# Optimization experiments

Measured on AMD Instinct MI355X. Metric: run time of the kernel, lower is better.

The kernel has to match this reference:

```python
import jax, jax.numpy as jnp
import numpy as np

N, E, G = 100000, 3200000, 5000
EPS = 1e-5
HEADS, HC = 8, 16


def setup_inputs() -> dict:
    key = jax.random.key(0)
    k = jax.random.split(key, 12)

    def lin(kk, fi, fo):
        return (jax.random.normal(kk, (fi, fo), jnp.float32) / np.sqrt(fi)).astype(jnp.float32)

    return {
        "x": jax.random.normal(k[0], (N, 20), jnp.float32),
        "edge_index": jax.random.randint(k[1], (2, E), 0, N, dtype=jnp.int32),
        "batch": jnp.sort(jax.random.randint(k[2], (N,), 0, G, dtype=jnp.int32)),
        "W1": lin(k[3], 20, 64), "b1": jnp.zeros((64,), jnp.float32),
        "g1": jnp.ones((64,), jnp.float32), "be1": jnp.zeros((64,), jnp.float32),
        "W2": lin(k[4], 64, 32), "b2": jnp.zeros((32,), jnp.float32),
        "g2": jnp.ones((32,), jnp.float32), "be2": jnp.zeros((32,), jnp.float32),
        "W3": lin(k[5], 32, 16), "b3": jnp.zeros((16,), jnp.float32),
        "g3": jnp.ones((16,), jnp.float32), "be3": jnp.zeros((16,), jnp.float32),
        "Wg": lin(k[6], 16, HEADS * HC),
        "att_src": jax.random.normal(k[7], (HEADS, HC), jnp.float32) * 0.1,
        "att_dst": jax.random.normal(k[8], (HEADS, HC), jnp.float32) * 0.1,
        "bg": jnp.zeros((HC,), jnp.float32),
        "Wf": lin(k[9], 16, 3), "bf": jnp.zeros((3,), jnp.float32),
    }


def reference(x, edge_index, batch,
              W1, b1, g1, be1, W2, b2, g2, be2, W3, b3, g3, be3,
              Wg, att_src, att_dst, bg, Wf, bf):
    src, dst = edge_index[0], edge_index[1]
    loop = jnp.arange(N, dtype=src.dtype)
    src_sl = jnp.concatenate([src, loop])  # self-loops (GCN + GAT add_self_loops)
    dst_sl = jnp.concatenate([dst, loop])

    # GCN symmetric normalization D^-1/2 (A+I) D^-1/2
    deg = jax.ops.segment_sum(jnp.ones_like(src_sl, dtype=jnp.float32), dst_sl, N)
    dinv = jnp.where(deg > 0, 1.0 / jnp.sqrt(deg), 0.0)
    norm = (dinv[src_sl] * dinv[dst_sl])[:, None]  # [E+N, 1]

    def gcn(h, W, b):
        h = h @ W
        return jax.ops.segment_sum(h[src_sl] * norm, dst_sl, N) + b

    def bn_relu(h, g, b):  # BatchNorm1d (train-mode batch stats) + ReLU
        mu = h.mean(0)
        var = ((h - mu) ** 2).mean(0)
        return jax.nn.relu(g * (h - mu) * jax.lax.rsqrt(var + EPS) + b)

    h = bn_relu(gcn(x, W1, b1), g1, be1)   # dropout = identity (eval)
    h = bn_relu(gcn(h, W2, b2), g2, be2)
    h = bn_relu(gcn(h, W3, b3), g3, be3)

    # GATConv: heads=8, concat=False (mean over heads), eval -> no dropout
    xg = (h @ Wg).reshape(N, HEADS, HC)
    a_src = (xg * att_src).sum(-1)  # [N, H]
    a_dst = (xg * att_dst).sum(-1)
    logit = jax.nn.leaky_relu(a_src[src_sl] + a_dst[dst_sl], 0.2)  # [E+N, H]
    m = jax.ops.segment_max(logit, dst_sl, N)          # segment softmax over dst
    e = jnp.exp(logit - m[dst_sl])
    s = jax.ops.segment_sum(e, dst_sl, N)
    alpha = e / s[dst_sl]
    agg = jax.ops.segment_sum(xg[src_sl] * alpha[:, :, None], dst_sl, N)  # [N,H,C]
    hg = agg.mean(1) + bg  # [N, 16]

    pooled = jax.ops.segment_sum(hg, batch, G)  # global_add_pool -> [G, 16]
    return pooled @ Wf + bf  # [G, 3]
```

## Files before the change

### kernel.cpp

```cpp
#include <hip/hip_runtime.h>
#include <hip/hip_fp16.h>

constexpr int NN = 100000;
constexpr int EE = 3200000;
constexpr int GG = 5000;
constexpr float BNEPS = 1e-5f;

constexpr int BINS = 128;
constexpr int NPB = (NN + BINS - 1) / BINS;
constexpr int BCHUNK = 8192;
constexpr int NBCH = (EE + BCHUNK - 1) / BCHUNK;
constexpr int BINCAP2 = 96;
constexpr int BINREG = 27648;
constexpr int LCAP = 26624;
constexpr int CTR_STRIDE = 32;

typedef int int4v __attribute__((ext_vector_type(4)));



__global__ __launch_bounds__(1024) void bin_edges(const int* __restrict__ ei,
                                                  unsigned* __restrict__ pairs,
                                                  int* __restrict__ binCur) {
    __shared__ int bcnt[BINS];
    __shared__ int bbase[BINS];
    __shared__ unsigned buf[BINS][BINCAP2];
    const int t = threadIdx.x;
    const int lane = t & 63, wv = t >> 6;
    for (int ch = blockIdx.x; ch < NBCH; ch += gridDim.x) {
        for (int k = t; k < BINS; k += 1024) bcnt[k] = 0;
        __syncthreads();
        const int qbase = ch * (BCHUNK / 4);
#pragma unroll
        for (int rep = 0; rep < 2; ++rep) {
            const int q = qbase + rep * 1024 + t;
            if (q < EE / 4) {
                int4v d = __builtin_nontemporal_load((const int4v*)(ei + EE) + q);
                int4v s = __builtin_nontemporal_load((const int4v*)ei + q);
                int dd[4] = {d.x, d.y, d.z, d.w};
                int ss[4] = {s.x, s.y, s.z, s.w};
#pragma unroll
                for (int k = 0; k < 4; ++k) {
                    int o = dd[k] / NPB;
                    unsigned pk = ((unsigned)(dd[k] - o * NPB) << 17) | (unsigned)ss[k];
                    int p = atomicAdd(&bcnt[o], 1);
                    if (p < BINCAP2) {
                        buf[o][p] = pk;
                    } else {
                        int gp = atomicAdd(&binCur[o * CTR_STRIDE], 1);
                        pairs[(size_t)o * BINREG + gp] = pk;
                    }
                }
            }
        }
        __syncthreads();
        if (t < BINS) {
            int c = bcnt[t] < BINCAP2 ? bcnt[t] : BINCAP2;
            bbase[t] = atomicAdd(&binCur[t * CTR_STRIDE], c);
            bcnt[t] = c;
        }
        __syncthreads();
        for (int o = wv; o < BINS; o += 16) {
            const int c = bcnt[o];
            const size_t base = (size_t)o * BINREG + bbase[o];
            for (int k = lane; k < c; k += 64) pairs[base + k] = buf[o][k];
        }
        __syncthreads();
    }
}


__global__ void bin_base(const int* __restrict__ binCur, int* __restrict__ binBase) {
    __shared__ int s[BINS];
    const int t = threadIdx.x;
    const int v = binCur[t * CTR_STRIDE];
    s[t] = v;
    __syncthreads();
    for (int off = 1; off < BINS; off <<= 1) {
        int add = (t >= off) ? s[t - off] : 0;
        __syncthreads();
        s[t] += add;
        __syncthreads();
    }
    binBase[t] = s[t] - v;
}


__global__ __launch_bounds__(1024) void scatter_lds(const unsigned* __restrict__ pairs,
                                                    const int* __restrict__ binCur,
                                                    const int* __restrict__ binBase,
                                                    int* __restrict__ rowptr,
                                                    float* __restrict__ dinv,
                                                    int* __restrict__ colA) {
    __shared__ int scnt[NPB];
    __shared__ int sscan[1024];
    __shared__ int lbuf[LCAP];
    const int b = blockIdx.x;
    const int t = threadIdx.x;
    const int lo = b * NPB;
    const int hi = (lo + NPB < NN) ? lo + NPB : NN;
    const int nb = hi - lo;
    const int tot = binCur[b * CTR_STRIDE];
    const int base = binBase[b];
    const unsigned* p = pairs + (size_t)b * BINREG;
    for (int k = t; k < nb; k += 1024) scnt[k] = 0;
    __syncthreads();
    for (int q = t; q < tot; q += 1024) atomicAdd(&scnt[p[q] >> 17], 1);
    __syncthreads();
    const int myc = (t < nb) ? scnt[t] : 0;
    sscan[t] = myc;
    __syncthreads();
    for (int off = 1; off < 1024; off <<= 1) {
        int add = (t >= off) ? sscan[t - off] : 0;
        __syncthreads();
        sscan[t] += add;
        __syncthreads();
    }
    const int excl = sscan[t] - myc;
    if (t < nb) {
        rowptr[lo + t] = base + excl;
        dinv[lo + t] = rsqrtf((float)(myc + 1));
        scnt[t] = excl;
    }
    if (b == BINS - 1 && t == 0) rowptr[NN] = base + tot;
    __syncthreads();
    for (int q = t; q < tot; q += 1024) {
        unsigned e = p[q];
        int pos = atomicAdd(&scnt[e >> 17], 1);
        int src = (int)(e & 0x1FFFFu);
        if (pos < LCAP) lbuf[pos] = src;
        else colA[base + pos] = src;
    }
    __syncthreads();
    const int m = tot < LCAP ? tot : LCAP;
    for (int k = t; k < m; k += 1024) colA[base + k] = lbuf[k];
}


__global__ void scale_x(const float* __restrict__ x, const float* __restrict__ dinv,
                        __half* __restrict__ xsc) {
    int idx = blockIdx.x * blockDim.x + threadIdx.x;
    if (idx < NN * 20) {
        int n = idx / 20;
        xsc[idx] = __float2half(x[idx] * dinv[n]);
    }
}


template <int FIN, int FOUT, bool AFFINE, bool SCALED, bool STATS, bool DUAL, bool SPLITOUT>
__global__ void gemm_k(const __half* __restrict__ hinA, const __half* __restrict__ hinB,
                       const float* __restrict__ sumsIn, const float* __restrict__ ssqIn,
                       const float* __restrict__ g, const float* __restrict__ be,
                       const float* __restrict__ W, const float* __restrict__ dinv,
                       const float* __restrict__ bias,
                       __half* __restrict__ outA, __half* __restrict__ outB,
                       float* __restrict__ sumsOut, float* __restrict__ ssqOut) {
    constexpr int NB = 256 / FOUT;
    __shared__ float Wl[FIN * FOUT];
    __shared__ float rows[NB][FIN];
    __shared__ float aa[AFFINE ? FIN : 1], bb[AFFINE ? FIN : 1];
    const int t = threadIdx.x;
    if constexpr (AFFINE) {
        if (t < FIN) {
            float mu = sumsIn[t] / (float)NN;
            float var = ssqIn[t] / (float)NN - mu * mu;
            float a = g[t] * rsqrtf(var + BNEPS);
            aa[t] = a;
            bb[t] = be[t] - mu * a;
        }
    }
    for (int i = t; i < FIN * FOUT; i += 256) Wl[i] = W[i];
    const int c = t % FOUT, s = t / FOUT;
    const int ngrp = (NN + NB - 1) / NB;
    float sAcc = 0.f, qAcc = 0.f;
    for (int grp = blockIdx.x; grp < ngrp; grp += gridDim.x) {
        __syncthreads();
        for (int i = t; i < NB * FIN; i += 256) {
            int sn = i / FIN, k = i % FIN;
            int n2 = grp * NB + sn;
            float v = 0.f;
            if (n2 < NN) {
                __half hv;
                if constexpr (DUAL) {
                    hv = (k < FIN / 2) ? hinA[(size_t)n2 * (FIN / 2) + k]
                                       : hinB[(size_t)n2 * (FIN / 2) + k - FIN / 2];
                } else {
                    hv = hinA[(size_t)n2 * FIN + k];
                }
                v = __half2float(hv);
                if constexpr (AFFINE) {
                    v = aa[k] * v + bb[k];
                    v = v > 0.f ? v : 0.f;
                }
            }
            rows[sn][k] = v;
        }
        __syncthreads();
        int node = grp * NB + s;
        if (node < NN) {
            float acc = 0.f;
#pragma unroll
            for (int k = 0; k < FIN; ++k) acc += rows[s][k] * Wl[k * FOUT + c];
            if constexpr (SCALED) {
                __half hv = __float2half(acc * dinv[node]);
                if constexpr (SPLITOUT) {
                    ((c < FOUT / 2) ? outA : outB)[(size_t)node * (FOUT / 2) + (c % (FOUT / 2))] = hv;
                } else {
                    outA[(size_t)node * FOUT + c] = hv;
                }
            } else {
                float val = acc + bias[c];
                outA[(size_t)node * FOUT + c] = __float2half(val);
                if constexpr (STATS) { sAcc += val; qAcc += val * val; }
            }
        }
    }
    if constexpr (STATS) {
        __shared__ float ls[FOUT], lq[FOUT];
        __syncthreads();
        if (t < FOUT) { ls[t] = 0.f; lq[t] = 0.f; }
        __syncthreads();
        atomicAdd(&ls[c], sAcc);
        atomicAdd(&lq[c], qAcc);
        __syncthreads();
        if (t < FOUT) { atomicAdd(&sumsOut[t], ls[t]); atomicAdd(&ssqOut[t], lq[t]); }
    }
}


template <int H2, int OUTF, bool STATS>
__global__ void agg_half(const __half2* __restrict__ src, const int* __restrict__ rowptr,
                         const int* __restrict__ colA, const float* __restrict__ dinv,
                         const float* __restrict__ bias, __half* __restrict__ out,
                         float* __restrict__ sumsOut, float* __restrict__ ssqOut) {
    constexpr int SUB = 64 / H2;
    const int lane = threadIdx.x & 63;
    const int wid = (blockIdx.x * blockDim.x + threadIdx.x) >> 6;
    const int totalWaves = (gridDim.x * blockDim.x) >> 6;
    const int f = lane % H2;
    const int sub = lane / H2;
    const int stride = totalWaves * SUB;
    float bx = 0.f, by = 0.f;
    if (bias != nullptr) {
        bx = bias[2 * f];
        by = bias[2 * f + 1];
    }
    const int i0 = (sub < SUB) ? wid * SUB + sub : NN;
    float sx = 0.f, qx = 0.f, sy = 0.f, qy = 0.f;
    for (int i = i0; i < NN; i += stride) {
        const int r0 = rowptr[i], r1 = rowptr[i + 1];
        float2 acc = __half22float2(src[(size_t)i * H2 + f]);
        float2 acc2 = {0.f, 0.f};
        int e = r0;
        for (; e + 3 < r1; e += 4) {
            int j0 = colA[e], j1 = colA[e + 1], j2 = colA[e + 2], j3 = colA[e + 3];
            float2 v0 = __half22float2(src[(size_t)j0 * H2 + f]);
            float2 v1 = __half22float2(src[(size_t)j1 * H2 + f]);
            float2 v2 = __half22float2(src[(size_t)j2 * H2 + f]);
            float2 v3 = __half22float2(src[(size_t)j3 * H2 + f]);
            acc.x += v0.x + v1.x;
            acc.y += v0.y + v1.y;
            acc2.x += v2.x + v3.x;
            acc2.y += v2.y + v3.y;
        }
        for (; e < r1; ++e) {
            float2 v = __half22float2(src[(size_t)colA[e] * H2 + f]);
            acc.x += v.x; acc.y += v.y;
        }
        acc.x += acc2.x; acc.y += acc2.y;
        const float d = dinv[i];
        float vx = d * acc.x + bx;
        float vy = d * acc.y + by;
        *(__half2*)(out + (size_t)i * OUTF + 2 * f) = __floats2half2_rn(vx, vy);
        if constexpr (STATS) { sx += vx; qx += vx * vx; sy += vy; qy += vy * vy; }
    }
    if constexpr (STATS) {
        __shared__ float ls[OUTF], lq[OUTF];
        const int t = threadIdx.x;
        if (t < OUTF) { ls[t] = 0.f; lq[t] = 0.f; }
        __syncthreads();
        atomicAdd(&ls[2 * f], sx);
        atomicAdd(&lq[2 * f], qx);
        atomicAdd(&ls[2 * f + 1], sy);
        atomicAdd(&lq[2 * f + 1], qy);
        __syncthreads();
        if (t < OUTF) { atomicAdd(&sumsOut[t], ls[t]); atomicAdd(&ssqOut[t], lq[t]); }
    }
}


__global__ void gat_mats(const float* __restrict__ Wg, const float* __restrict__ att_src,
                         const float* __restrict__ att_dst, const float* __restrict__ Wf,
                         const float* __restrict__ bg, float* __restrict__ Psrc,
                         float* __restrict__ Pdst, float* __restrict__ M,
                         float* __restrict__ bgW) {
    int t = threadIdx.x;
    if (t < 128) {
        int k = t >> 3, h = t & 7;
        float s = 0.f, d = 0.f;
        for (int c = 0; c < 16; ++c) {
            float wv = Wg[k * 128 + h * 16 + c];
            s += wv * att_src[h * 16 + c];
            d += wv * att_dst[h * 16 + c];
        }
        Psrc[k * 8 + h] = s;
        Pdst[k * 8 + h] = d;
    } else if (t < 512) {
        int m = t - 128;
        if (m < 384) {
            int hk = m / 3, j = m - hk * 3;
            int H = hk >> 4, k = hk & 15;
            float s = 0.f;
            for (int c = 0; c < 16; ++c) s += Wg[k * 128 + H * 16 + c] * Wf[c * 3 + j];
            M[hk * 3 + j] = 0.125f * s;
        }
    } else if (t < 515) {
        int j = t - 512;
        float s = 0.f;
        for (int c = 0; c < 16; ++c) s += bg[c] * Wf[c * 3 + j];
        bgW[j] = s;
    }
}


__global__ void gat_pre2(const __half* __restrict__ h3,
                         const float* __restrict__ sums3, const float* __restrict__ ssq3,
                         const float* __restrict__ g3, const float* __restrict__ be3,
                         const float* __restrict__ Psrc, const float* __restrict__ Pdst,
                         float4* __restrict__ zas, float* __restrict__ adst) {
    __shared__ float Ps[128], Pd[128], aa[16], bb[16];
    int t = threadIdx.x;
    if (t < 128) { Ps[t] = Psrc[t]; Pd[t] = Pdst[t]; }
    if (t < 16) {
        float mu = sums3[t] / (float)NN;
        float var = ssq3[t] / (float)NN - mu * mu;
        float a = g3[t] * rsqrtf(var + BNEPS);
        aa[t] = a;
        bb[t] = be3[t] - mu * a;
    }
    __syncthreads();
    int n = blockIdx.x * blockDim.x + t;
    if (n >= NN) return;
    union { float4 f4[2]; __half2 h2v[8]; } u;
    const float4* hp = (const float4*)(h3 + (size_t)n * 16);
    u.f4[0] = hp[0];
    u.f4[1] = hp[1];
    float zv[16];
#pragma unroll
    for (int k = 0; k < 8; ++k) {
        float2 p = __half22float2(u.h2v[k]);
        float v0 = aa[2 * k] * p.x + bb[2 * k];
        float v1 = aa[2 * k + 1] * p.y + bb[2 * k + 1];
        zv[2 * k] = v0 > 0.f ? v0 : 0.f;
        zv[2 * k + 1] = v1 > 0.f ? v1 : 0.f;
    }
    __half2 zh[8];
#pragma unroll
    for (int k = 0; k < 8; ++k) zh[k] = __floats2half2_rn(zv[2 * k], zv[2 * k + 1]);
    float as[8], ad[8];
#pragma unroll
    for (int h = 0; h < 8; ++h) { as[h] = 0.f; ad[h] = 0.f; }
#pragma unroll
    for (int k = 0; k < 16; ++k) {
        float zk = zv[k];
#pragma unroll
        for (int h = 0; h < 8; ++h) {
            as[h] += zk * Ps[k * 8 + h];
            ad[h] += zk * Pd[k * 8 + h];
        }
    }
    float4* zrow = zas + (size_t)n * 4;
    zrow[0] = ((float4*)zh)[0];
    zrow[1] = ((float4*)zh)[1];
    zrow[2] = make_float4(as[0], as[1], as[2], as[3]);
    zrow[3] = make_float4(as[4], as[5], as[6], as[7]);
    float4* d4 = (float4*)(adst + (size_t)n * 8);
    d4[0] = make_float4(ad[0], ad[1], ad[2], ad[3]);
    d4[1] = make_float4(ad[4], ad[5], ad[6], ad[7]);
}


__device__ __forceinline__ float leaky02(float x) { return x > 0.f ? x : 0.2f * x; }

__global__ void gat_agg7(const float4* __restrict__ zas, const float* __restrict__ adst,
                         const int* __restrict__ rowptr, const int* __restrict__ colA,
                         const int* __restrict__ batch, const float* __restrict__ Mg,
                         float* __restrict__ out) {
    __shared__ float Ml[384];
    for (int k = threadIdx.x; k < 384; k += 256) Ml[k] = Mg[k];
    __syncthreads();
    const int lane = threadIdx.x & 63;
    const int ls = lane & 7;
    const int q = ls & 3;
    const int hh = ls >> 2;
    const int grp = lane >> 3;
    const int gb = lane & 56;
    const int wid = (blockIdx.x * blockDim.x + threadIdx.x) >> 6;
    const int totalWaves = (gridDim.x * blockDim.x) >> 6;
    const int stride = totalWaves * 8;
    const char* zb = (const char*)zas;
    for (int i = wid * 8 + grp; i < NN; i += stride) {
        const int r0 = rowptr[i], r1 = rowptr[i + 1];
        const float adv = __builtin_nontemporal_load(adst + (size_t)i * 8 + ls);
        float acc[4][4];
        float wsum[4];
#pragma unroll
        for (int h = 0; h < 4; ++h) {
            wsum[h] = 0.f;
#pragma unroll
            for (int k = 0; k < 4; ++k) acc[h][k] = 0.f;
        }
        auto compute = [&](float av, float2 zr, bool val) {
            const __half2* zp = (const __half2*)&zr;
            const float2 f0 = __half22float2(zp[0]), f1 = __half22float2(zp[1]);
            const float zf[4] = {f0.x, f0.y, f1.x, f1.y};
            const float w = val ? __expf(leaky02(av + adv)) : 0.f;
            float wq[4];
#pragma unroll
            for (int h = 0; h < 4; ++h) wq[h] = __shfl(w, gb + hh * 4 + h);
#pragma unroll
            for (int h = 0; h < 4; ++h) {
                wsum[h] += wq[h];
#pragma unroll
                for (int k = 0; k < 4; ++k) acc[h][k] += wq[h] * zf[k];
            }
        };
        int e = r0;
        int jA = i, jB = i;
        bool vB = false;
        if (e < r1) { jB = colA[e]; ++e; vB = true; }
        const char* rowA = zb + (size_t)jA * 64;
        const char* rowB = zb + (size_t)jB * 64;
        float avA = *(const float*)(rowA + 32 + ls * 4);
        float2 zA = *(const float2*)(rowA + q * 8);
        float avB = *(const float*)(rowB + 32 + ls * 4);
        float2 zB = *(const float2*)(rowB + q * 8);
        while (true) {
            int jA2 = i, jB2 = i;
            bool vA2 = false, vB2 = false;
            if (e < r1) { jA2 = colA[e]; ++e; vA2 = true; }
            if (e < r1) { jB2 = colA[e]; ++e; vB2 = true; }
            const char* rA2 = zb + (size_t)jA2 * 64;
            const char* rB2 = zb + (size_t)jB2 * 64;
            float avA2 = *(const float*)(rA2 + 32 + ls * 4);
            float2 zA2 = *(const float2*)(rA2 + q * 8);
            float avB2 = *(const float*)(rB2 + 32 + ls * 4);
            float2 zB2 = *(const float2*)(rB2 + q * 8);
            compute(avA, zA, true);
            compute(avB, zB, vB);
            if (!vA2) break;
            avA = avA2; zA = zA2; avB = avB2; zB = zB2; vB = vB2;
        }
        float o0 = 0.f, o1 = 0.f, o2 = 0.f;
#pragma unroll
        for (int h = 0; h < 4; ++h) {
            const float inv = 1.f / wsum[h];
            const int hk0 = (hh * 4 + h) * 16 + q * 4;
#pragma unroll
            for (int k = 0; k < 4; ++k) {
                const float v = acc[h][k] * inv;
                const float* m = &Ml[(hk0 + k) * 3];
                o0 += v * m[0];
                o1 += v * m[1];
                o2 += v * m[2];
            }
        }
#pragma unroll
        for (int off = 1; off < 8; off <<= 1) {
            o0 += __shfl_xor(o0, off);
            o1 += __shfl_xor(o1, off);
            o2 += __shfl_xor(o2, off);
        }
        const int g = batch[i];
        if (ls < 3) {
            const float ov = (ls == 0) ? o0 : (ls == 1) ? o1 : o2;
            atomicAdd(&out[g * 3 + ls], ov);
        }
    }
}


__global__ void graph_bounds(const int* __restrict__ batch, int* __restrict__ gstart) {
    int n = blockIdx.x * blockDim.x + threadIdx.x;
    if (n < NN) {
        int bn = batch[n];
        int bp = (n == 0) ? -1 : batch[n - 1];
        for (int g = bp + 1; g <= bn; ++g) gstart[g] = n;
        if (n == NN - 1)
            for (int g = bn + 1; g <= GG; ++g) gstart[g] = NN;
    }
}


__global__ void pool_init(const int* __restrict__ gstart, const float* __restrict__ bgW,
                          const float* __restrict__ bf, float* __restrict__ out) {
    int g = blockIdx.x * blockDim.x + threadIdx.x;
    if (g < GG) {
        float cnt = (float)(gstart[g + 1] - gstart[g]);
#pragma unroll
        for (int j = 0; j < 3; ++j) out[g * 3 + j] = cnt * bgW[j] + bf[j];
    }
}


extern "C" void kernel_launch(void* const* d_in, const int* in_sizes, int n_in,
                              void* d_out, int out_size, void* d_ws, size_t ws_size,
                              hipStream_t stream) {
    const float* x = (const float*)d_in[0];
    const int* ei = (const int*)d_in[1];
    const int* batch = (const int*)d_in[2];
    const float* W1 = (const float*)d_in[3];  const float* b1 = (const float*)d_in[4];
    const float* g1 = (const float*)d_in[5];  const float* be1 = (const float*)d_in[6];
    const float* W2 = (const float*)d_in[7];  const float* b2 = (const float*)d_in[8];
    const float* g2 = (const float*)d_in[9];  const float* be2 = (const float*)d_in[10];
    const float* W3 = (const float*)d_in[11]; const float* b3 = (const float*)d_in[12];
    const float* g3 = (const float*)d_in[13]; const float* be3 = (const float*)d_in[14];
    const float* Wg = (const float*)d_in[15];
    const float* att_src = (const float*)d_in[16];
    const float* att_dst = (const float*)d_in[17];
    const float* bg = (const float*)d_in[18];
    const float* Wf = (const float*)d_in[19];
    const float* bf = (const float*)d_in[20];
    float* out = (float*)d_out;

    char* w = (char*)d_ws;
    auto alloc = [&](size_t bytes) -> char* {
        char* p = w;
        w += (bytes + 255) & ~(size_t)255;
        return p;
    };
    int* binCur = (int*)alloc((size_t)BINS * CTR_STRIDE * 4);
    float* sums1 = (float*)alloc(64 * 4); float* ssq1 = (float*)alloc(64 * 4);
    float* sums2 = (float*)alloc(32 * 4); float* ssq2 = (float*)alloc(32 * 4);
    float* sums3 = (float*)alloc(16 * 4); float* ssq3 = (float*)alloc(16 * 4);
    size_t zeroBytes = (size_t)(w - (char*)d_ws);
    int* binBase = (int*)alloc((size_t)BINS * 4);
    float* Psrc = (float*)alloc(128 * 4);
    float* Pdst = (float*)alloc(128 * 4);
    float* Mm = (float*)alloc(384 * 4);
    float* bgW = (float*)alloc(3 * 4);
    int* gstart = (int*)alloc((size_t)(GG + 1) * 4);
    int* rowptr = (int*)alloc((size_t)(NN + 1) * 4);
    int* colA = (int*)alloc((size_t)EE * 4);
    float* dinv = (float*)alloc((size_t)NN * 4);
    char* A = alloc((size_t)NN * 64 * 4);
    char* B = alloc((size_t)NN * 64 * 4);

    unsigned* pairs = (unsigned*)A;
    __half* xsc  = (__half*)B;
    __half* aggx = (__half*)(B + (size_t)NN * 64);
    __half* h1   = (__half*)A;
    __half* hs2a = (__half*)B;
    __half* hs2b = (__half*)(B + (size_t)NN * 32);
    __half* h2a  = (__half*)(B + (size_t)NN * 64);
    __half* h2b  = (__half*)(B + (size_t)NN * 96);
    __half* hs3  = (__half*)A;
    __half* h3   = (__half*)(A + (size_t)NN * 32);
    char*   zas  = A + (size_t)NN * 96;
    float*  adst = (float*)(A + (size_t)NN * 160);

    hipMemsetAsync(d_ws, 0, zeroBytes, stream);

    bin_edges<<<256, 1024, 0, stream>>>(ei, pairs, binCur);
    bin_base<<<1, BINS, 0, stream>>>(binCur, binBase);
    scatter_lds<<<BINS, 1024, 0, stream>>>(pairs, binCur, binBase, rowptr, dinv, colA);
    gat_mats<<<1, 1024, 0, stream>>>(Wg, att_src, att_dst, Wf, bg, Psrc, Pdst, Mm, bgW);
    graph_bounds<<<(NN + 255) / 256, 256, 0, stream>>>(batch, gstart);
    pool_init<<<(GG + 255) / 256, 256, 0, stream>>>(gstart, bgW, bf, out);

    scale_x<<<(NN * 20 + 255) / 256, 256, 0, stream>>>(x, dinv, xsc);
    agg_half<10, 20, false><<<2048, 256, 0, stream>>>((const __half2*)xsc, rowptr, colA, dinv,
                                                      nullptr, aggx, nullptr, nullptr);
    gemm_k<20, 64, false, false, true, false, false><<<2048, 256, 0, stream>>>(
        aggx, nullptr, nullptr, nullptr, nullptr, nullptr, W1, dinv, b1, h1, nullptr,
        sums1, ssq1);

    gemm_k<64, 32, true, true, false, false, true><<<2048, 256, 0, stream>>>(
        h1, nullptr, sums1, ssq1, g1, be1, W2, dinv, nullptr, hs2a, hs2b, nullptr, nullptr);
    agg_half<8, 16, true><<<2048, 256, 0, stream>>>((const __half2*)hs2a, rowptr, colA, dinv,
                                                    b2, h2a, sums2, ssq2);
    agg_half<8, 16, true><<<2048, 256, 0, stream>>>((const __half2*)hs2b, rowptr, colA, dinv,
                                                    b2 + 16, h2b, sums2 + 16, ssq2 + 16);

    gemm_k<32, 16, true, true, false, true, false><<<2048, 256, 0, stream>>>(
        h2a, h2b, sums2, ssq2, g2, be2, W3, dinv, nullptr, hs3, nullptr, nullptr, nullptr);
    agg_half<8, 16, true><<<2048, 256, 0, stream>>>((const __half2*)hs3, rowptr, colA, dinv,
                                                    b3, h3, sums3, ssq3);

    gat_pre2<<<(NN + 255) / 256, 256, 0, stream>>>(h3, sums3, ssq3, g3, be3, Psrc, Pdst,
                                                   (float4*)zas, adst);
    gat_agg7<<<3200, 256, 0, stream>>>((const float4*)zas, adst, rowptr, colA, batch, Mm, out);
}
```

Baseline: 493.8 us.

## Recompute GAT attention scores per edge and add nontemporal loads and stores

```diff
diff --git a/kernel.cpp b/kernel.cpp
--- a/kernel.cpp
+++ b/kernel.cpp
@@ -16,6 +16,20 @@
 constexpr int CTR_STRIDE = 32;
 
 typedef int int4v __attribute__((ext_vector_type(4)));
+typedef float f32x4 __attribute__((ext_vector_type(4)));
+
+static __device__ __forceinline__ __half ntload_h(const __half* p) {
+    unsigned short u = __builtin_nontemporal_load((const unsigned short*)p);
+    __half h; __builtin_memcpy(&h, &u, 2); return h;
+}
+static __device__ __forceinline__ void ntstore_h(__half* p, __half v) {
+    unsigned short u; __builtin_memcpy(&u, &v, 2);
+    __builtin_nontemporal_store(u, (unsigned short*)p);
+}
+static __device__ __forceinline__ void ntstore_h2(__half* p, __half2 v) {
+    unsigned u; __builtin_memcpy(&u, &v, 4);
+    __builtin_nontemporal_store(u, (unsigned*)p);
+}
 
 
 
@@ -63,7 +77,8 @@
         for (int o = wv; o < BINS; o += 16) {
             const int c = bcnt[o];
             const size_t base = (size_t)o * BINREG + bbase[o];
-            for (int k = lane; k < c; k += 64) pairs[base + k] = buf[o][k];
+            for (int k = lane; k < c; k += 64)
+                __builtin_nontemporal_store(buf[o][k], pairs + base + k);
         }
         __syncthreads();
     }
@@ -105,7 +120,8 @@
     const unsigned* p = pairs + (size_t)b * BINREG;
     for (int k = t; k < nb; k += 1024) scnt[k] = 0;
     __syncthreads();
-    for (int q = t; q < tot; q += 1024) atomicAdd(&scnt[p[q] >> 17], 1);
+    for (int q = t; q < tot; q += 1024)
+        atomicAdd(&scnt[__builtin_nontemporal_load(p + q) >> 17], 1);
     __syncthreads();
     const int myc = (t < nb) ? scnt[t] : 0;
     sscan[t] = myc;
@@ -133,7 +149,8 @@
     }
     __syncthreads();
     const int m = tot < LCAP ? tot : LCAP;
-    for (int k = t; k < m; k += 1024) colA[base + k] = lbuf[k];
+    for (int k = t; k < m; k += 1024)
+        __builtin_nontemporal_store(lbuf[k], colA + base + k);
 }
 
 
@@ -142,7 +159,7 @@
     int idx = blockIdx.x * blockDim.x + threadIdx.x;
     if (idx < NN * 20) {
         int n = idx / 20;
-        xsc[idx] = __float2half(x[idx] * dinv[n]);
+        ntstore_h(xsc + idx, __float2half(x[idx] * dinv[n]));
     }
 }
 
@@ -182,10 +199,10 @@
             if (n2 < NN) {
                 __half hv;
                 if constexpr (DUAL) {
-                    hv = (k < FIN / 2) ? hinA[(size_t)n2 * (FIN / 2) + k]
-                                       : hinB[(size_t)n2 * (FIN / 2) + k - FIN / 2];
+                    hv = (k < FIN / 2) ? ntload_h(hinA + (size_t)n2 * (FIN / 2) + k)
+                                       : ntload_h(hinB + (size_t)n2 * (FIN / 2) + k - FIN / 2);
                 } else {
-                    hv = hinA[(size_t)n2 * FIN + k];
+                    hv = ntload_h(hinA + (size_t)n2 * FIN + k);
                 }
                 v = __half2float(hv);
                 if constexpr (AFFINE) {
@@ -204,13 +221,15 @@
             if constexpr (SCALED) {
                 __half hv = __float2half(acc * dinv[node]);
                 if constexpr (SPLITOUT) {
-                    ((c < FOUT / 2) ? outA : outB)[(size_t)node * (FOUT / 2) + (c % (FOUT / 2))] = hv;
+                    ntstore_h(((c < FOUT / 2) ? outA : outB) +
+                                  (size_t)node * (FOUT / 2) + (c % (FOUT / 2)),
+                              hv);
                 } else {
-                    outA[(size_t)node * FOUT + c] = hv;
+                    ntstore_h(outA + (size_t)node * FOUT + c, hv);
                 }
             } else {
                 float val = acc + bias[c];
-                outA[(size_t)node * FOUT + c] = __float2half(val);
+                ntstore_h(outA + (size_t)node * FOUT + c, __float2half(val));
                 if constexpr (STATS) { sAcc += val; qAcc += val * val; }
             }
         }
@@ -253,7 +272,10 @@
         float2 acc2 = {0.f, 0.f};
         int e = r0;
         for (; e + 3 < r1; e += 4) {
-            int j0 = colA[e], j1 = colA[e + 1], j2 = colA[e + 2], j3 = colA[e + 3];
+            int j0 = __builtin_nontemporal_load(colA + e);
+            int j1 = __builtin_nontemporal_load(colA + e + 1);
+            int j2 = __builtin_nontemporal_load(colA + e + 2);
+            int j3 = __builtin_nontemporal_load(colA + e + 3);
             float2 v0 = __half22float2(src[(size_t)j0 * H2 + f]);
             float2 v1 = __half22float2(src[(size_t)j1 * H2 + f]);
             float2 v2 = __half22float2(src[(size_t)j2 * H2 + f]);
@@ -264,14 +286,15 @@
             acc2.y += v2.y + v3.y;
         }
         for (; e < r1; ++e) {
-            float2 v = __half22float2(src[(size_t)colA[e] * H2 + f]);
+            int j = __builtin_nontemporal_load(colA + e);
+            float2 v = __half22float2(src[(size_t)j * H2 + f]);
             acc.x += v.x; acc.y += v.y;
         }
         acc.x += acc2.x; acc.y += acc2.y;
         const float d = dinv[i];
         float vx = d * acc.x + bx;
         float vy = d * acc.y + by;
-        *(__half2*)(out + (size_t)i * OUTF + 2 * f) = __floats2half2_rn(vx, vy);
+        ntstore_h2(out + (size_t)i * OUTF + 2 * f, __floats2half2_rn(vx, vy));
         if constexpr (STATS) { sx += vx; qx += vx * vx; sy += vy; qy += vy * vy; }
     }
     if constexpr (STATS) {
@@ -323,14 +346,12 @@
 }
 
 
-__global__ void gat_pre2(const __half* __restrict__ h3,
+__global__ void gat_prez(const __half* __restrict__ h3,
                          const float* __restrict__ sums3, const float* __restrict__ ssq3,
                          const float* __restrict__ g3, const float* __restrict__ be3,
-                         const float* __restrict__ Psrc, const float* __restrict__ Pdst,
-                         float4* __restrict__ zas, float* __restrict__ adst) {
-    __shared__ float Ps[128], Pd[128], aa[16], bb[16];
+                         __half* __restrict__ z) {
+    __shared__ float aa[16], bb[16];
     int t = threadIdx.x;
-    if (t < 128) { Ps[t] = Psrc[t]; Pd[t] = Pdst[t]; }
     if (t < 16) {
         float mu = sums3[t] / (float)NN;
         float var = ssq3[t] / (float)NN - mu * mu;
@@ -345,125 +366,107 @@
     const float4* hp = (const float4*)(h3 + (size_t)n * 16);
     u.f4[0] = hp[0];
     u.f4[1] = hp[1];
-    float zv[16];
+    __half2 zh[8];
 #pragma unroll
     for (int k = 0; k < 8; ++k) {
         float2 p = __half22float2(u.h2v[k]);
         float v0 = aa[2 * k] * p.x + bb[2 * k];
         float v1 = aa[2 * k + 1] * p.y + bb[2 * k + 1];
-        zv[2 * k] = v0 > 0.f ? v0 : 0.f;
-        zv[2 * k + 1] = v1 > 0.f ? v1 : 0.f;
-    }
-    __half2 zh[8];
-#pragma unroll
-    for (int k = 0; k < 8; ++k) zh[k] = __floats2half2_rn(zv[2 * k], zv[2 * k + 1]);
-    float as[8], ad[8];
-#pragma unroll
-    for (int h = 0; h < 8; ++h) { as[h] = 0.f; ad[h] = 0.f; }
-#pragma unroll
-    for (int k = 0; k < 16; ++k) {
-        float zk = zv[k];
-#pragma unroll
-        for (int h = 0; h < 8; ++h) {
-            as[h] += zk * Ps[k * 8 + h];
-            ad[h] += zk * Pd[k * 8 + h];
-        }
-    }
-    float4* zrow = zas + (size_t)n * 4;
-    zrow[0] = ((float4*)zh)[0];
-    zrow[1] = ((float4*)zh)[1];
-    zrow[2] = make_float4(as[0], as[1], as[2], as[3]);
-    zrow[3] = make_float4(as[4], as[5], as[6], as[7]);
-    float4* d4 = (float4*)(adst + (size_t)n * 8);
-    d4[0] = make_float4(ad[0], ad[1], ad[2], ad[3]);
-    d4[1] = make_float4(ad[4], ad[5], ad[6], ad[7]);
+        zh[k] = __floats2half2_rn(v0 > 0.f ? v0 : 0.f, v1 > 0.f ? v1 : 0.f);
+    }
+    f32x4* zo = (f32x4*)(z + (size_t)n * 16);
+    __builtin_nontemporal_store(((const f32x4*)zh)[0], zo);
+    __builtin_nontemporal_store(((const f32x4*)zh)[1], zo + 1);
 }
 
 
 __device__ __forceinline__ float leaky02(float x) { return x > 0.f ? x : 0.2f * x; }
 
-__global__ void gat_agg7(const float4* __restrict__ zas, const float* __restrict__ adst,
-                         const int* __restrict__ rowptr, const int* __restrict__ colA,
-                         const int* __restrict__ batch, const float* __restrict__ Mg,
-                         float* __restrict__ out) {
+__global__ void gat_agg8(const float4* __restrict__ z4, const int* __restrict__ rowptr,
+                         const int* __restrict__ colA, const int* __restrict__ batch,
+                         const float* __restrict__ Psrc, const float* __restrict__ Pdst,
+                         const float* __restrict__ Mg, float* __restrict__ out) {
     __shared__ float Ml[384];
-    for (int k = threadIdx.x; k < 384; k += 256) Ml[k] = Mg[k];
+    __shared__ float Pdl[128];
+    {
+        const int t = threadIdx.x;
+        for (int k = t; k < 384; k += 256) Ml[k] = Mg[k];
+        if (t < 128) Pdl[t] = Pdst[t];
+    }
     __syncthreads();
     const int lane = threadIdx.x & 63;
     const int ls = lane & 7;
-    const int q = ls & 3;
-    const int hh = ls >> 2;
     const int grp = lane >> 3;
-    const int gb = lane & 56;
     const int wid = (blockIdx.x * blockDim.x + threadIdx.x) >> 6;
     const int totalWaves = (gridDim.x * blockDim.x) >> 6;
     const int stride = totalWaves * 8;
-    const char* zb = (const char*)zas;
+    float PsR[16];
+#pragma unroll
+    for (int k = 0; k < 16; ++k) PsR[k] = Psrc[k * 8 + ls];
     for (int i = wid * 8 + grp; i < NN; i += stride) {
         const int r0 = rowptr[i], r1 = rowptr[i + 1];
-        const float adv = __builtin_nontemporal_load(adst + (size_t)i * 8 + ls);
-        float acc[4][4];
-        float wsum[4];
-#pragma unroll
-        for (int h = 0; h < 4; ++h) {
-            wsum[h] = 0.f;
-#pragma unroll
-            for (int k = 0; k < 4; ++k) acc[h][k] = 0.f;
-        }
-        auto compute = [&](float av, float2 zr, bool val) {
-            const __half2* zp = (const __half2*)&zr;
-            const float2 f0 = __half22float2(zp[0]), f1 = __half22float2(zp[1]);
-            const float zf[4] = {f0.x, f0.y, f1.x, f1.y};
-            const float w = val ? __expf(leaky02(av + adv)) : 0.f;
-            float wq[4];
-#pragma unroll
-            for (int h = 0; h < 4; ++h) wq[h] = __shfl(w, gb + hh * 4 + h);
-#pragma unroll
-            for (int h = 0; h < 4; ++h) {
-                wsum[h] += wq[h];
-#pragma unroll
-                for (int k = 0; k < 4; ++k) acc[h][k] += wq[h] * zf[k];
+        float4 c0 = z4[(size_t)i * 2], c1 = z4[(size_t)i * 2 + 1];
+        int e = r0;
+        int jn = (e < r1) ? __builtin_nontemporal_load(colA + e) : i;
+        float4 n0 = z4[(size_t)jn * 2], n1 = z4[(size_t)jn * 2 + 1];
+        float zf[16];
+        {
+            const __half2* ha = (const __half2*)&c0;
+            const __half2* hb = (const __half2*)&c1;
+#pragma unroll
+            for (int p = 0; p < 4; ++p) {
+                float2 a = __half22float2(ha[p]);
+                zf[2 * p] = a.x; zf[2 * p + 1] = a.y;
+                float2 b = __half22float2(hb[p]);
+                zf[8 + 2 * p] = b.x; zf[8 + 2 * p + 1] = b.y;
             }
-        };
-        int e = r0;
-        int jA = i, jB = i;
-        bool vB = false;
-        if (e < r1) { jB = colA[e]; ++e; vB = true; }
-        const char* rowA = zb + (size_t)jA * 64;
-        const char* rowB = zb + (size_t)jB * 64;
-        float avA = *(const float*)(rowA + 32 + ls * 4);
-        float2 zA = *(const float2*)(rowA + q * 8);
-        float avB = *(const float*)(rowB + 32 + ls * 4);
-        float2 zB = *(const float2*)(rowB + q * 8);
-        while (true) {
-            int jA2 = i, jB2 = i;
-            bool vA2 = false, vB2 = false;
-            if (e < r1) { jA2 = colA[e]; ++e; vA2 = true; }
-            if (e < r1) { jB2 = colA[e]; ++e; vB2 = true; }
-            const char* rA2 = zb + (size_t)jA2 * 64;
-            const char* rB2 = zb + (size_t)jB2 * 64;
-            float avA2 = *(const float*)(rA2 + 32 + ls * 4);
-            float2 zA2 = *(const float2*)(rA2 + q * 8);
-            float avB2 = *(const float*)(rB2 + 32 + ls * 4);
-            float2 zB2 = *(const float2*)(rB2 + q * 8);
-            compute(avA, zA, true);
-            compute(avB, zB, vB);
-            if (!vA2) break;
-            avA = avA2; zA = zA2; avB = avB2; zB = zB2; vB = vB2;
-        }
+        }
+        float as = 0.f, ad = 0.f;
+#pragma unroll
+        for (int k = 0; k < 16; ++k) {
+            as += zf[k] * PsR[k];
+            ad += zf[k] * Pdl[k * 8 + ls];
+        }
+        const float adv = ad;
+        float w = __expf(leaky02(as + adv));
+        float ws = w;
+        float acc[16];
+#pragma unroll
+        for (int k = 0; k < 16; ++k) acc[k] = w * zf[k];
+        while (e < r1) {
+            c0 = n0; c1 = n1;
+            const int e2 = e + 1;
+            jn = (e2 < r1) ? __builtin_nontemporal_load(colA + e2) : i;
+            n0 = z4[(size_t)jn * 2]; n1 = z4[(size_t)jn * 2 + 1];
+            {
+                const __half2* ha = (const __half2*)&c0;
+                const __half2* hb = (const __half2*)&c1;
+#pragma unroll
+                for (int p = 0; p < 4; ++p) {
+                    float2 a = __half22float2(ha[p]);
+                    zf[2 * p] = a.x; zf[2 * p + 1] = a.y;
+                    float2 b = __half22float2(hb[p]);
+                    zf[8 + 2 * p] = b.x; zf[8 + 2 * p + 1] = b.y;
+                }
+            }
+            float a2 = 0.f;
+#pragma unroll
+            for (int k = 0; k < 16; ++k) a2 += zf[k] * PsR[k];
+            w = __expf(leaky02(a2 + adv));
+            ws += w;
+#pragma unroll
+            for (int k = 0; k < 16; ++k) acc[k] += w * zf[k];
+            e = e2;
+        }
+        const float inv = 1.f / ws;
         float o0 = 0.f, o1 = 0.f, o2 = 0.f;
 #pragma unroll
-        for (int h = 0; h < 4; ++h) {
-            const float inv = 1.f / wsum[h];
-            const int hk0 = (hh * 4 + h) * 16 + q * 4;
-#pragma unroll
-            for (int k = 0; k < 4; ++k) {
-                const float v = acc[h][k] * inv;
-                const float* m = &Ml[(hk0 + k) * 3];
-                o0 += v * m[0];
-                o1 += v * m[1];
-                o2 += v * m[2];
-            }
+        for (int k = 0; k < 16; ++k) {
+            const float v = acc[k] * inv;
+            const float* m = &Ml[(ls * 16 + k) * 3];
+            o0 += v * m[0];
+            o1 += v * m[1];
+            o2 += v * m[2];
         }
 #pragma unroll
         for (int off = 1; off < 8; off <<= 1) {
@@ -556,8 +559,7 @@
     __half* h2b  = (__half*)(B + (size_t)NN * 96);
     __half* hs3  = (__half*)A;
     __half* h3   = (__half*)(A + (size_t)NN * 32);
-    char*   zas  = A + (size_t)NN * 96;
-    float*  adst = (float*)(A + (size_t)NN * 160);
+    __half* z    = (__half*)(A + (size_t)NN * 64);
 
     hipMemsetAsync(d_ws, 0, zeroBytes, stream);
 
@@ -587,7 +589,7 @@
     agg_half<8, 16, true><<<2048, 256, 0, stream>>>((const __half2*)hs3, rowptr, colA, dinv,
                                                     b3, h3, sums3, ssq3);
 
-    gat_pre2<<<(NN + 255) / 256, 256, 0, stream>>>(h3, sums3, ssq3, g3, be3, Psrc, Pdst,
-                                                   (float4*)zas, adst);
-    gat_agg7<<<3200, 256, 0, stream>>>((const float4*)zas, adst, rowptr, colA, batch, Mm, out);
-}
+    gat_prez<<<(NN + 255) / 256, 256, 0, stream>>>(h3, sums3, ssq3, g3, be3, z);
+    gat_agg8<<<3200, 256, 0, stream>>>((const float4*)z, rowptr, colA, batch, Psrc, Pdst,
+                                       Mm, out);
+}
```

After: 606.0 us. 22.7% more time.

## Merge split layer-2 aggregation into one 32-wide pass; nontemporal column loads

Applied to the files above, without the earlier changes.

```diff
diff --git a/kernel.cpp b/kernel.cpp
--- a/kernel.cpp
+++ b/kernel.cpp
@@ -16,6 +16,7 @@
 constexpr int CTR_STRIDE = 32;
 
 typedef int int4v __attribute__((ext_vector_type(4)));
+typedef _Float16 f16x8 __attribute__((ext_vector_type(8)));
 
 
 
@@ -147,13 +148,13 @@
 }
 
 
-template <int FIN, int FOUT, bool AFFINE, bool SCALED, bool STATS, bool DUAL, bool SPLITOUT>
-__global__ void gemm_k(const __half* __restrict__ hinA, const __half* __restrict__ hinB,
+template <int FIN, int FOUT, bool AFFINE, bool SCALED, bool STATS>
+__global__ void gemm_k(const __half* __restrict__ hin,
                        const float* __restrict__ sumsIn, const float* __restrict__ ssqIn,
                        const float* __restrict__ g, const float* __restrict__ be,
                        const float* __restrict__ W, const float* __restrict__ dinv,
                        const float* __restrict__ bias,
-                       __half* __restrict__ outA, __half* __restrict__ outB,
+                       __half* __restrict__ out,
                        float* __restrict__ sumsOut, float* __restrict__ ssqOut) {
     constexpr int NB = 256 / FOUT;
     __shared__ float Wl[FIN * FOUT];
@@ -180,14 +181,7 @@
             int n2 = grp * NB + sn;
             float v = 0.f;
             if (n2 < NN) {
-                __half hv;
-                if constexpr (DUAL) {
-                    hv = (k < FIN / 2) ? hinA[(size_t)n2 * (FIN / 2) + k]
-                                       : hinB[(size_t)n2 * (FIN / 2) + k - FIN / 2];
-                } else {
-                    hv = hinA[(size_t)n2 * FIN + k];
-                }
-                v = __half2float(hv);
+                v = __half2float(hin[(size_t)n2 * FIN + k]);
                 if constexpr (AFFINE) {
                     v = aa[k] * v + bb[k];
                     v = v > 0.f ? v : 0.f;
@@ -202,15 +196,10 @@
 #pragma unroll
             for (int k = 0; k < FIN; ++k) acc += rows[s][k] * Wl[k * FOUT + c];
             if constexpr (SCALED) {
-                __half hv = __float2half(acc * dinv[node]);
-                if constexpr (SPLITOUT) {
-                    ((c < FOUT / 2) ? outA : outB)[(size_t)node * (FOUT / 2) + (c % (FOUT / 2))] = hv;
-                } else {
-                    outA[(size_t)node * FOUT + c] = hv;
-                }
+                out[(size_t)node * FOUT + c] = __float2half(acc * dinv[node]);
             } else {
                 float val = acc + bias[c];
-                outA[(size_t)node * FOUT + c] = __float2half(val);
+                out[(size_t)node * FOUT + c] = __float2half(val);
                 if constexpr (STATS) { sAcc += val; qAcc += val * val; }
             }
         }
@@ -253,7 +242,10 @@
         float2 acc2 = {0.f, 0.f};
         int e = r0;
         for (; e + 3 < r1; e += 4) {
-            int j0 = colA[e], j1 = colA[e + 1], j2 = colA[e + 2], j3 = colA[e + 3];
+            int j0 = __builtin_nontemporal_load(colA + e);
+            int j1 = __builtin_nontemporal_load(colA + e + 1);
+            int j2 = __builtin_nontemporal_load(colA + e + 2);
+            int j3 = __builtin_nontemporal_load(colA + e + 3);
             float2 v0 = __half22float2(src[(size_t)j0 * H2 + f]);
             float2 v1 = __half22float2(src[(size_t)j1 * H2 + f]);
             float2 v2 = __half22float2(src[(size_t)j2 * H2 + f]);
@@ -264,7 +256,8 @@
             acc2.y += v2.y + v3.y;
         }
         for (; e < r1; ++e) {
-            float2 v = __half22float2(src[(size_t)colA[e] * H2 + f]);
+            int j = __builtin_nontemporal_load(colA + e);
+            float2 v = __half22float2(src[(size_t)j * H2 + f]);
             acc.x += v.x; acc.y += v.y;
         }
         acc.x += acc2.x; acc.y += acc2.y;
@@ -341,22 +334,22 @@
     __syncthreads();
     int n = blockIdx.x * blockDim.x + t;
     if (n >= NN) return;
-    union { float4 f4[2]; __half2 h2v[8]; } u;
-    const float4* hp = (const float4*)(h3 + (size_t)n * 16);
-    u.f4[0] = hp[0];
-    u.f4[1] = hp[1];
+    const f16x8* hp = (const f16x8*)(h3 + (size_t)n * 16);
+    f16x8 v0 = hp[0], v1 = hp[1];
     float zv[16];
 #pragma unroll
     for (int k = 0; k < 8; ++k) {
-        float2 p = __half22float2(u.h2v[k]);
-        float v0 = aa[2 * k] * p.x + bb[2 * k];
-        float v1 = aa[2 * k + 1] * p.y + bb[2 * k + 1];
-        zv[2 * k] = v0 > 0.f ? v0 : 0.f;
-        zv[2 * k + 1] = v1 > 0.f ? v1 : 0.f;
-    }
-    __half2 zh[8];
-#pragma unroll
-    for (int k = 0; k < 8; ++k) zh[k] = __floats2half2_rn(zv[2 * k], zv[2 * k + 1]);
+        float a0 = aa[k] * (float)v0[k] + bb[k];
+        float a1 = aa[8 + k] * (float)v1[k] + bb[8 + k];
+        zv[k] = a0 > 0.f ? a0 : 0.f;
+        zv[8 + k] = a1 > 0.f ? a1 : 0.f;
+    }
+    f16x8 zh0, zh1;
+#pragma unroll
+    for (int k = 0; k < 8; ++k) {
+        zh0[k] = (_Float16)zv[k];
+        zh1[k] = (_Float16)zv[8 + k];
+    }
     float as[8], ad[8];
 #pragma unroll
     for (int h = 0; h < 8; ++h) { as[h] = 0.f; ad[h] = 0.f; }
@@ -369,9 +362,10 @@
             ad[h] += zk * Pd[k * 8 + h];
         }
     }
+    f16x8* zrow16 = (f16x8*)(zas + (size_t)n * 4);
+    zrow16[0] = zh0;
+    zrow16[1] = zh1;
     float4* zrow = zas + (size_t)n * 4;
-    zrow[0] = ((float4*)zh)[0];
-    zrow[1] = ((float4*)zh)[1];
     zrow[2] = make_float4(as[0], as[1], as[2], as[3]);
     zrow[3] = make_float4(as[4], as[5], as[6], as[7]);
     float4* d4 = (float4*)(adst + (size_t)n * 8);
@@ -550,10 +544,8 @@
     __half* xsc  = (__half*)B;
     __half* aggx = (__half*)(B + (size_t)NN * 64);
     __half* h1   = (__half*)A;
-    __half* hs2a = (__half*)B;
-    __half* hs2b = (__half*)(B + (size_t)NN * 32);
-    __half* h2a  = (__half*)(B + (size_t)NN * 64);
-    __half* h2b  = (__half*)(B + (size_t)NN * 96);
+    __half* hs2  = (__half*)B;
+    __half* h2   = (__half*)(B + (size_t)NN * 64);
     __half* hs3  = (__half*)A;
     __half* h3   = (__half*)(A + (size_t)NN * 32);
     char*   zas  = A + (size_t)NN * 96;
@@ -571,19 +563,16 @@
     scale_x<<<(NN * 20 + 255) / 256, 256, 0, stream>>>(x, dinv, xsc);
     agg_half<10, 20, false><<<2048, 256, 0, stream>>>((const __half2*)xsc, rowptr, colA, dinv,
                                                       nullptr, aggx, nullptr, nullptr);
-    gemm_k<20, 64, false, false, true, false, false><<<2048, 256, 0, stream>>>(
-        aggx, nullptr, nullptr, nullptr, nullptr, nullptr, W1, dinv, b1, h1, nullptr,
-        sums1, ssq1);
-
-    gemm_k<64, 32, true, true, false, false, true><<<2048, 256, 0, stream>>>(
-        h1, nullptr, sums1, ssq1, g1, be1, W2, dinv, nullptr, hs2a, hs2b, nullptr, nullptr);
-    agg_half<8, 16, true><<<2048, 256, 0, stream>>>((const __half2*)hs2a, rowptr, colA, dinv,
-                                                    b2, h2a, sums2, ssq2);
-    agg_half<8, 16, true><<<2048, 256, 0, stream>>>((const __half2*)hs2b, rowptr, colA, dinv,
-                                                    b2 + 16, h2b, sums2 + 16, ssq2 + 16);
-
-    gemm_k<32, 16, true, true, false, true, false><<<2048, 256, 0, stream>>>(
-        h2a, h2b, sums2, ssq2, g2, be2, W3, dinv, nullptr, hs3, nullptr, nullptr, nullptr);
+    gemm_k<20, 64, false, false, true><<<2048, 256, 0, stream>>>(
+        aggx, nullptr, nullptr, nullptr, nullptr, W1, dinv, b1, h1, sums1, ssq1);
+
+    gemm_k<64, 32, true, true, false><<<2048, 256, 0, stream>>>(
+        h1, sums1, ssq1, g1, be1, W2, dinv, nullptr, hs2, nullptr, nullptr);
+    agg_half<16, 32, true><<<2048, 256, 0, stream>>>((const __half2*)hs2, rowptr, colA, dinv,
+                                                     b2, h2, sums2, ssq2);
+
+    gemm_k<32, 16, true, true, false><<<2048, 256, 0, stream>>>(
+        h2, sums2, ssq2, g2, be2, W3, dinv, nullptr, hs3, nullptr, nullptr);
     agg_half<8, 16, true><<<2048, 256, 0, stream>>>((const __half2*)hs3, rowptr, colA, dinv,
                                                     b3, h3, sums3, ssq3);
 
```

Result: no change. 500.0 us (+1.3%).
